# Performance work log

Hardware: AMD Instinct MI355X
Metric: run time of the kernel (lower is better)

The kernel has to match this reference:

```python
import jax, jax.numpy as jnp
import numpy as np

OUT = 7      # roi_align output_size
RATIO = 2    # fixed sampling_ratio (torchvision default -1 is adaptive; fixed 2 used for jit-ability)
IMG = 518    # image size (DINOv2 patch 14 -> 37x37 feature grid)


def setup_inputs() -> dict:
    key = jax.random.key(0)
    ks = jax.random.split(key, 12)
    B, N, C, H, W = 4, 512, 256, 37, 37
    NUM_CLASSES = 91
    f0 = jax.random.normal(ks[0], (B, C, H, W), jnp.float32)
    f1 = jax.random.normal(ks[1], (B, C, H, W), jnp.float32)
    f2 = jax.random.normal(ks[2], (B, C, H, W), jnp.float32)
    f3 = jax.random.normal(ks[3], (B, C, H, W), jnp.float32)
    # proposals in image coords so areas span all 4 level buckets (32^2..128^2+)
    cx = jax.random.uniform(ks[4], (B, N)) * IMG
    cy = jax.random.uniform(ks[5], (B, N)) * IMG
    bw = jax.random.uniform(ks[6], (B, N)) * 248.0 + 8.0
    bh = jax.random.uniform(ks[7], (B, N)) * 248.0 + 8.0
    x1 = jnp.maximum(cx - 0.5 * bw, 0.0)
    y1 = jnp.maximum(cy - 0.5 * bh, 0.0)
    x2 = jnp.minimum(cx + 0.5 * bw, float(IMG))
    y2 = jnp.minimum(cy + 0.5 * bh, float(IMG))
    proposals = jnp.stack([x1, y1, x2, y2], axis=-1)  # [B,N,4]
    D = C * OUT * OUT  # 12544
    w1 = jax.random.normal(ks[8], (D, 1024), jnp.float32) * 0.02
    b1 = jnp.zeros((1024,), jnp.float32)
    w2 = jax.random.normal(ks[9], (1024, 1024), jnp.float32) * 0.02
    b2 = jnp.zeros((1024,), jnp.float32)
    wc = jax.random.normal(ks[10], (1024, NUM_CLASSES), jnp.float32) * 0.02
    bc = jnp.zeros((NUM_CLASSES,), jnp.float32)
    wb = jax.random.normal(ks[11], (1024, 4), jnp.float32) * 0.02
    bb = jnp.zeros((4,), jnp.float32)
    return {"f0": f0, "f1": f1, "f2": f2, "f3": f3, "proposals": proposals,
            "w1": w1, "b1": b1, "w2": w2, "b2": b2,
            "wc": wc, "bc": bc, "wb": wb, "bb": bb}


def _multilevel_roi_align(f0, f1, f2, f3, proposals):
    B, C, H, W = f0.shape
    N = proposals.shape[1]
    P = OUT * RATIO * OUT * RATIO
    # levels stacked along spatial axis: [B, C, 4*H*W]
    feats_cat = jnp.stack([f0, f1, f2, f3], axis=2).reshape(B, C, 4 * H * W)
    bw = proposals[..., 2] - proposals[..., 0]
    bh = proposals[..., 3] - proposals[..., 1]
    area = bw * bh
    # area-based FPN level: <32^2->0, <64^2->1, <128^2->2, else 3
    lvl = ((area >= 32.0 ** 2).astype(jnp.int32)
           + (area >= 64.0 ** 2).astype(jnp.int32)
           + (area >= 128.0 ** 2).astype(jnp.int32))  # [B,N]
    # roi_align, spatial_scale=1.0, aligned=True
    x1 = proposals[..., 0] - 0.5
    y1 = proposals[..., 1] - 0.5
    bin_w = bw / OUT
    bin_h = bh / OUT
    offs = jnp.arange(OUT, dtype=jnp.float32)[:, None] + (jnp.arange(RATIO, dtype=jnp.float32) + 0.5)[None, :] / RATIO  # [7,2]
    ys = y1[..., None, None] + offs * bin_h[..., None, None]  # [B,N,7,2]
    xs = x1[..., None, None] + offs * bin_w[..., None, None]  # [B,N,7,2]
    y = ys[..., :, :, None, None]  # [B,N,7,2,1,1]
    x = xs[..., None, None, :, :]  # [B,N,1,1,7,2]
    valid = ((y >= -1.0) & (y <= H) & (x >= -1.0) & (x <= W)).astype(f0.dtype)
    yc = jnp.clip(y, 0.0, H - 1.0)
    xc = jnp.clip(x, 0.0, W - 1.0)
    y0f = jnp.floor(yc)
    x0f = jnp.floor(xc)
    y0 = y0f.astype(jnp.int32)
    x0 = x0f.astype(jnp.int32)
    y1i = jnp.minimum(y0 + 1, H - 1)
    x1i = jnp.minimum(x0 + 1, W - 1)
    ly = yc - y0f
    lx = xc - x0f
    hy = 1.0 - ly
    hx = 1.0 - lx
    base = (lvl * (H * W))[:, :, None, None, None, None]
    shp = (B, N, OUT, RATIO, OUT, RATIO)

    def gather(yi, xi):
        idx = jnp.broadcast_to(base + yi * W + xi, shp).reshape(B, N * P)
        return jax.vmap(lambda fb, ib: jnp.take(fb, ib, axis=1))(feats_cat, idx)  # [B,C,N*P]

    def wflat(w):
        return jnp.broadcast_to(w * valid, shp).reshape(B, 1, N * P)

    acc = (wflat(hy * hx) * gather(y0, x0)
           + wflat(hy * lx) * gather(y0, x1i)
           + wflat(ly * hx) * gather(y1i, x0)
           + wflat(ly * lx) * gather(y1i, x1i))
    roi = acc.reshape(B, C, N, OUT, RATIO, OUT, RATIO).sum(axis=(4, 6)) / (RATIO * RATIO)
    return roi.transpose(0, 2, 1, 3, 4)  # [B,N,C,7,7]


def reference(f0, f1, f2, f3, proposals, w1, b1, w2, b2, wc, bc, wb, bb):
    B, N = proposals.shape[0], proposals.shape[1]
    roi = _multilevel_roi_align(f0, f1, f2, f3, proposals)  # [B,N,C,7,7]
    flat = roi.reshape(B * N, -1)  # torch flatten order matches [C,7,7]
    h1 = jax.nn.relu(flat @ w1 + b1)
    h2 = jax.nn.relu(h1 @ w2 + b2)
    scores = (h2 @ wc + bc).reshape(B, N, -1)
    bbox_deltas = (h2 @ wb + bb).reshape(B, N, 4)
    return scores, bbox_deltas
```

## Files before the change

kernel.cpp:

```cpp
#include <hip/hip_runtime.h>
#include <hip/hip_bf16.h>
#include <stdint.h>

#define FH 37
#define FW 37
#define FC 256
#define NB 4
#define NP 512
#define BNT (NB*NP)
#define KDIM (FC*49)
#define HID 1024
#define NHEAD 95
#define CAP 256

typedef __bf16 bf16x8 __attribute__((ext_vector_type(8)));
typedef float  f32x4  __attribute__((ext_vector_type(4)));

__global__ __launch_bounds__(256) void k_transpose(const float* __restrict__ f0,
                                                   const float* __restrict__ f1,
                                                   const float* __restrict__ f2,
                                                   const float* __restrict__ f3,
                                                   float* __restrict__ ft) {
  __shared__ float tile[32][33];
  int bl = blockIdx.z;
  int b = bl >> 2, l = bl & 3;
  const float* src = (l == 0 ? f0 : l == 1 ? f1 : l == 2 ? f2 : f3) + (size_t)b * FC * FH * FW;
  int yx0 = blockIdx.x * 32;
  int c0  = blockIdx.y * 32;
  int tx = threadIdx.x;
  int ty = threadIdx.y;
  #pragma unroll
  for (int i = 0; i < 32; i += 8) {
    int c  = c0 + ty + i;
    int yx = yx0 + tx;
    float v = (yx < FH * FW) ? src[(size_t)c * (FH * FW) + yx] : 0.f;
    tile[ty + i][tx] = v;
  }
  __syncthreads();
  #pragma unroll
  for (int i = 0; i < 32; i += 8) {
    int yx = yx0 + ty + i;
    int c  = c0 + tx;
    if (yx < FH * FW)
      ft[((size_t)bl * (FH * FW) + yx) * FC + c] = tile[tx][ty + i];
  }
}

__global__ __launch_bounds__(256) void k_compact(const float* __restrict__ props,
                                                 int* __restrict__ count,
                                                 int* __restrict__ list) {
  int bn = blockIdx.x * 256 + threadIdx.x;
  float px1 = props[(size_t)bn * 4 + 0];
  float py1 = props[(size_t)bn * 4 + 1];
  float px2 = props[(size_t)bn * 4 + 2];
  float py2 = props[(size_t)bn * 4 + 3];
  float bw = px2 - px1, bh = py2 - py1;
  float X1 = px1 - 0.5f, Y1 = py1 - 0.5f;
  float binw = bw * (1.f / 7.f), binh = bh * (1.f / 7.f);
  float sy0 = Y1 + ((float)0 * 0.5f + 0.25f) * binh;
  float sx0 = X1 + ((float)0 * 0.5f + 0.25f) * binw;
  bool active = (sy0 <= 37.f) && (sx0 <= 37.f);
  if (active) {
    int s = atomicAdd(count, 1);
    if (s < CAP) list[s] = bn;
  }
}

__global__ __launch_bounds__(256) void k_roi(const float* __restrict__ ft,
                                             const float* __restrict__ props,
                                             const int* __restrict__ count,
                                             const int* __restrict__ list,
                                             __hip_bfloat16* __restrict__ Ahi,
                                             __hip_bfloat16* __restrict__ Alo) {
  int s = blockIdx.x;
  int cnt = min(*count, CAP);
  if (s >= cnt) return;
  int bn = list[s];
  int b = bn >> 9;
  int p = blockIdx.y;
  int oy = p / 7, ox = p % 7;
  int c = threadIdx.x;

  float px1 = props[(size_t)bn * 4 + 0];
  float py1 = props[(size_t)bn * 4 + 1];
  float px2 = props[(size_t)bn * 4 + 2];
  float py2 = props[(size_t)bn * 4 + 3];
  float bw = px2 - px1, bh = py2 - py1;
  float area = bw * bh;
  int lvl = (area >= 1024.f) + (area >= 4096.f) + (area >= 16384.f);
  float X1 = px1 - 0.5f, Y1 = py1 - 0.5f;
  float binw = bw * (1.f / 7.f), binh = bh * (1.f / 7.f);
  int fbase = ((b * 4 + lvl) * (FH * FW)) * FC;

  float acc = 0.f;
  #pragma unroll
  for (int ry = 0; ry < 2; ++ry) {
    int iy = oy * 2 + ry;
    float sy = Y1 + ((float)iy * 0.5f + 0.25f) * binh;
    #pragma unroll
    for (int rx = 0; rx < 2; ++rx) {
      int ix = ox * 2 + rx;
      float sx = X1 + ((float)ix * 0.5f + 0.25f) * binw;
      float valid = (sy >= -1.f && sy <= 37.f && sx >= -1.f && sx <= 37.f) ? 0.25f : 0.f;
      float yc = fminf(fmaxf(sy, 0.f), 36.f);
      float xc = fminf(fmaxf(sx, 0.f), 36.f);
      float y0f = floorf(yc), x0f = floorf(xc);
      int y0 = (int)y0f, x0 = (int)x0f;
      int y1i = min(y0 + 1, 36), x1i = min(x0 + 1, 36);
      float ly = yc - y0f, lx = xc - x0f;
      float hy = 1.f - ly, hx = 1.f - lx;
      float w00 = hy * hx * valid, w01 = hy * lx * valid;
      float w10 = ly * hx * valid, w11 = ly * lx * valid;
      if (w00 != 0.f) acc += w00 * ft[fbase + (y0  * FW + x0 ) * FC + c];
      if (w01 != 0.f) acc += w01 * ft[fbase + (y0  * FW + x1i) * FC + c];
      if (w10 != 0.f) acc += w10 * ft[fbase + (y1i * FW + x0 ) * FC + c];
      if (w11 != 0.f) acc += w11 * ft[fbase + (y1i * FW + x1i) * FC + c];
    }
  }
  size_t o = (size_t)s * KDIM + p * FC + c;
  __hip_bfloat16 h = __float2bfloat16(acc);
  Ahi[o] = h;
  Alo[o] = __float2bfloat16(acc - __bfloat162float(h));
}

__global__ __launch_bounds__(256, 2) void k_gemm_fused(
    const __hip_bfloat16* __restrict__ Ahi,
    const __hip_bfloat16* __restrict__ Alo,
    const float* __restrict__ Wf,
    float* __restrict__ part,
    const int* __restrict__ countPtr,
    int Kt, int kChunk, int reorder) {
  int cnt = min(*countPtr, CAP);
  if ((int)blockIdx.x * 128 >= cnt) return;
  __shared__ __align__(16) char lds[49152];
  const int t = threadIdx.x, lane = t & 63, wave = t >> 6;
  const int m0 = blockIdx.x * 128, n0 = blockIdx.y * 64;
  const int kStart = blockIdx.z * kChunk;
  const int niters = kChunk >> 5;

  const int nn = t & 63;
  const int q2 = t >> 6;
  const size_t rstep = reorder ? (size_t)(49 * HID) : (size_t)HID;

  const int wm = (wave & 1) * 64, wn2 = (wave >> 1) * 32;
  const int rsel = lane & 15, q = lane >> 4;

  f32x4 acc[4][2];
  #pragma unroll
  for (int m = 0; m < 4; ++m)
    #pragma unroll
    for (int n = 0; n < 2; ++n)
      acc[m][n] = (f32x4){0.f, 0.f, 0.f, 0.f};

  auto loadB = [&](float* v, int k0) {
    size_t rb0 = reorder ? (size_t)((k0 & 255) * 49 + (k0 >> 8)) : (size_t)k0;
    const float* p = Wf + rb0 * HID + (size_t)(q2 * 8) * rstep + n0 + nn;
    #pragma unroll
    for (int j = 0; j < 8; ++j) v[j] = p[(size_t)j * rstep];
  };

  auto writeB = [&](int buf, const float* v) {
    bf16x8 hv, lv;
    #pragma unroll
    for (int e = 0; e < 8; ++e) {
      float f = v[e];
      __hip_bfloat16 h = __float2bfloat16(f);
      float fr = f - __bfloat162float(h);
      __hip_bfloat16 l2 = __float2bfloat16(fr);
      hv[e] = *reinterpret_cast<__bf16*>(&h);
      lv[e] = *reinterpret_cast<__bf16*>(&l2);
    }
    char* bh = lds + buf * 24576 + 16384 + nn * 64 + ((q2 ^ (nn & 3)) << 4);
    *(bf16x8*)bh = hv;
    *(bf16x8*)(bh + 4096) = lv;
  };

  auto stageA = [&](int buf, int k0) {
    #pragma unroll
    for (int pl = 0; pl < 2; ++pl) {
      const __hip_bfloat16* src = pl ? Alo : Ahi;
      #pragma unroll
      for (int i = 0; i < 2; ++i) {
        int seg = wave * 2 + i;
        int row = seg * 16 + (lane >> 2);
        int cq = (lane & 3) ^ (row & 3);
        const char* g = (const char*)(src + (size_t)(m0 + row) * Kt + k0 + cq * 8);
        char* l = lds + buf * 24576 + pl * 8192 + seg * 1024;
        __builtin_amdgcn_global_load_lds((const unsigned int __attribute__((address_space(1)))*)g,
                                         (unsigned int __attribute__((address_space(3)))*)l,
                                         16, 0, 0);
      }
    }
  };

  auto compute = [&](int buf) {
    const char* base = lds + buf * 24576;
    bf16x8 ah[4], al2[4], bh2[2], bl2[2];
    #pragma unroll
    for (int mf = 0; mf < 4; ++mf) {
      int row = wm + mf * 16 + rsel;
      int off = row * 64 + ((q ^ (row & 3)) << 4);
      ah[mf]  = *(const bf16x8*)(base + off);
      al2[mf] = *(const bf16x8*)(base + 8192 + off);
    }
    #pragma unroll
    for (int nf = 0; nf < 2; ++nf) {
      int col = wn2 + nf * 16 + rsel;
      int off = col * 64 + ((q ^ (col & 3)) << 4);
      bh2[nf] = *(const bf16x8*)(base + 16384 + off);
      bl2[nf] = *(const bf16x8*)(base + 20480 + off);
    }
    #pragma unroll
    for (int mf = 0; mf < 4; ++mf)
      #pragma unroll
      for (int nf = 0; nf < 2; ++nf) {
        acc[mf][nf] = __builtin_amdgcn_mfma_f32_16x16x32_bf16(ah[mf],  bh2[nf], acc[mf][nf], 0, 0, 0);
        acc[mf][nf] = __builtin_amdgcn_mfma_f32_16x16x32_bf16(ah[mf],  bl2[nf], acc[mf][nf], 0, 0, 0);
        acc[mf][nf] = __builtin_amdgcn_mfma_f32_16x16x32_bf16(al2[mf], bh2[nf], acc[mf][nf], 0, 0, 0);
      }
  };

  float vA[8], vB[8];
  loadB(vA, kStart);
  stageA(0, kStart);
  writeB(0, vA);
  __syncthreads();

  int k = kStart;
  const int npair = niters >> 1;
  for (int pr = 0; pr < npair; ++pr) {
    loadB(vB, k + 32);
    stageA(1, k + 32);
    compute(0);
    writeB(1, vB);
    __syncthreads();
    bool more = (pr + 1 < npair);
    if (more) {
      loadB(vA, k + 64);
      stageA(0, k + 64);
    }
    compute(1);
    if (more) writeB(0, vA);
    __syncthreads();
    k += 64;
  }

  float* pbase = part + (size_t)blockIdx.z * (CAP * HID);
  #pragma unroll
  for (int mf = 0; mf < 4; ++mf)
    #pragma unroll
    for (int nf = 0; nf < 2; ++nf) {
      int row = m0 + wm + mf * 16 + q * 4;
      int col = n0 + wn2 + nf * 16 + rsel;
      #pragma unroll
      for (int r = 0; r < 4; ++r)
        pbase[(size_t)(row + r) * HID + col] = acc[mf][nf][r];
    }
}

__global__ __launch_bounds__(256) void k_reduce1(const float* __restrict__ part,
                                                 const float* __restrict__ bias,
                                                 const int* __restrict__ countPtr,
                                                 int S,
                                                 __hip_bfloat16* __restrict__ Hhi,
                                                 __hip_bfloat16* __restrict__ Hlo) {
  int cnt = min(*countPtr, CAP);
  if ((int)(blockIdx.x >> 2) >= cnt) return;
  size_t i = (size_t)blockIdx.x * 256 + threadIdx.x;
  const size_t tot = (size_t)CAP * HID;
  int col = (int)(i & (HID - 1));
  float a = bias[col];
  for (int s = 0; s < S; ++s) a += part[(size_t)s * tot + i];
  a = fmaxf(a, 0.f);
  __hip_bfloat16 h = __float2bfloat16(a);
  Hhi[i] = h;
  Hlo[i] = __float2bfloat16(a - __bfloat162float(h));
}

__global__ __launch_bounds__(256) void k_h2c(const float* __restrict__ w2,
                                             const float* __restrict__ b1,
                                             float* __restrict__ h2cr) {
  int n = blockIdx.x * 256 + threadIdx.x;
  int k0 = blockIdx.y * 128;
  float acc = 0.f;
  for (int k = k0; k < k0 + 128; ++k)
    acc += fmaxf(b1[k], 0.f) * w2[(size_t)k * HID + n];
  atomicAdd(&h2cr[n], acc);
}

__global__ __launch_bounds__(256) void k_outc(const float* __restrict__ h2cr,
                                              const float* __restrict__ b2,
                                              const float* __restrict__ wc,
                                              const float* __restrict__ bc,
                                              const float* __restrict__ wb,
                                              const float* __restrict__ bb,
                                              float* __restrict__ outc) {
  __shared__ float red[4];
  int j = blockIdx.x;
  int t = threadIdx.x;
  float acc = 0.f;
  for (int n = t; n < HID; n += 256) {
    float h = fmaxf(b2[n] + h2cr[n], 0.f);
    float w = (j < 91) ? wc[(size_t)n * 91 + j] : wb[(size_t)n * 4 + (j - 91)];
    acc += h * w;
  }
  #pragma unroll
  for (int o = 32; o; o >>= 1) acc += __shfl_down(acc, o, 64);
  if ((t & 63) == 0) red[t >> 6] = acc;
  __syncthreads();
  if (t == 0) {
    float bj = (j < 91) ? bc[j] : bb[j - 91];
    outc[j] = bj + red[0] + red[1] + red[2] + red[3];
  }
}

__global__ __launch_bounds__(256) void k_fill(const float* __restrict__ outc,
                                              float* __restrict__ out) {
  int i = blockIdx.x * 256 + threadIdx.x;
  const int SC = BNT * 91;
  if (i < SC) out[i] = outc[i % 91];
  else {
    int r = i - SC;
    if (r < BNT * 4) out[SC + r] = outc[91 + (r & 3)];
  }
}

__global__ __launch_bounds__(256) void k_head(const float* __restrict__ part,
                                              const float* __restrict__ b2,
                                              const float* __restrict__ wc,
                                              const float* __restrict__ bc,
                                              const float* __restrict__ wb,
                                              const float* __restrict__ bb,
                                              const int* __restrict__ count,
                                              const int* __restrict__ list,
                                              float* __restrict__ out) {
  __shared__ float row[HID];
  int s = blockIdx.x;
  int cnt = min(*count, CAP);
  if (s >= cnt) return;
  int bn = list[s];
  int t = threadIdx.x;
  const size_t tot = (size_t)CAP * HID;
  #pragma unroll
  for (int j = 0; j < 4; ++j) {
    int col = t + j * 256;
    float a = b2[col];
    #pragma unroll
    for (int ss = 0; ss < 8; ++ss) a += part[(size_t)ss * tot + (size_t)s * HID + col];
    row[col] = fmaxf(a, 0.f);
  }
  __syncthreads();
  if (t < NHEAD) {
    float acc = (t < 91) ? bc[t] : bb[t - 91];
    if (t < 91) {
      for (int k = 0; k < HID; ++k) acc += row[k] * wc[(size_t)k * 91 + t];
      out[(size_t)bn * 91 + t] = acc;
    } else {
      for (int k = 0; k < HID; ++k) acc += row[k] * wb[(size_t)k * 4 + (t - 91)];
      out[(size_t)BNT * 91 + (size_t)bn * 4 + (t - 91)] = acc;
    }
  }
}

extern "C" void kernel_launch(void* const* d_in, const int* in_sizes, int n_in,
                              void* d_out, int out_size, void* d_ws, size_t ws_size,
                              hipStream_t stream) {
  const float* f0    = (const float*)d_in[0];
  const float* f1    = (const float*)d_in[1];
  const float* f2    = (const float*)d_in[2];
  const float* f3    = (const float*)d_in[3];
  const float* props = (const float*)d_in[4];
  const float* w1    = (const float*)d_in[5];
  const float* b1    = (const float*)d_in[6];
  const float* w2    = (const float*)d_in[7];
  const float* b2    = (const float*)d_in[8];
  const float* wc    = (const float*)d_in[9];
  const float* bc    = (const float*)d_in[10];
  const float* wb    = (const float*)d_in[11];
  const float* bb    = (const float*)d_in[12];
  float* out = (float*)d_out;

  char* ws = (char*)d_ws;
  size_t off = 0;
  auto alloc = [&](size_t bytes) -> char* {
    char* p = ws + off;
    off += (bytes + 255) & ~(size_t)255;
    return p;
  };
  float*          ft    = (float*)         alloc((size_t)16 * FH * FW * FC * 4);
  __hip_bfloat16* Ahi   = (__hip_bfloat16*)alloc((size_t)CAP * KDIM * 2);
  __hip_bfloat16* Alo   = (__hip_bfloat16*)alloc((size_t)CAP * KDIM * 2);
  float*          part  = (float*)         alloc((size_t)28 * CAP * HID * 4);
  __hip_bfloat16* H1hi  = (__hip_bfloat16*)alloc((size_t)CAP * HID * 2);
  __hip_bfloat16* H1lo  = (__hip_bfloat16*)alloc((size_t)CAP * HID * 2);
  float*          h2cr  = (float*)         alloc(HID * 4);
  int*            count = (int*)           alloc(256);
  int*            list  = (int*)           alloc(CAP * 4);
  float*          outc  = (float*)         alloc(NHEAD * 4);
  (void)ws_size; (void)in_sizes; (void)n_in; (void)out_size;

  hipMemsetAsync(h2cr, 0, HID * 4 + 256, stream);

  k_transpose<<<dim3(43, 8, 16), dim3(32, 8), 0, stream>>>(f0, f1, f2, f3, ft);
  k_compact<<<8, 256, 0, stream>>>(props, count, list);
  k_roi<<<dim3(CAP, 49), 256, 0, stream>>>(ft, props, count, list, Ahi, Alo);

  k_h2c<<<dim3(4, 8), 256, 0, stream>>>(w2, b1, h2cr);
  k_outc<<<NHEAD, 256, 0, stream>>>(h2cr, b2, wc, bc, wb, bb, outc);
  k_fill<<<760, 256, 0, stream>>>(outc, out);

  k_gemm_fused<<<dim3(CAP / 128, 16, 28), 256, 0, stream>>>(Ahi, Alo, w1, part, count,
                                                            KDIM, 448, 1);
  k_reduce1<<<CAP * HID / 256, 256, 0, stream>>>(part, b1, count, 28, H1hi, H1lo);
  k_gemm_fused<<<dim3(CAP / 128, 16, 8), 256, 0, stream>>>(H1hi, H1lo, w2, part, count,
                                                           HID, 128, 0);
  k_head<<<CAP, 256, 0, stream>>>(part, b2, wc, bc, wb, bb, count, list, out);
}
```

Measured before the change: 240.3 us.

## Store ROI features in channel-major order and widen GEMM N-tile to 128

The ROI kernel now writes activations in [C,49] flatten order, so the first GEMM reads w1 rows contiguously and drops the strided reorder indexing of B loads. The GEMM block tile grows from 128x64 to 128x128, with each wave computing a 64x64 sub-tile and LDS doubled to 64KB. This halves the number of N blocks and raises A reuse per block, but it increases register pressure (16 accumulators, 16-value B prefetch) and LDS use, which may lower occupancy.

Measured after the change: 237.1 us. About the same (-1.4%).

```diff
diff --git a/kernel.cpp b/kernel.cpp
--- a/kernel.cpp
+++ b/kernel.cpp
@@ -117,7 +117,7 @@
       if (w11 != 0.f) acc += w11 * ft[fbase + (y1i * FW + x1i) * FC + c];
     }
   }
-  size_t o = (size_t)s * KDIM + p * FC + c;
+  size_t o = (size_t)s * KDIM + (size_t)c * 49 + p;
   __hip_bfloat16 h = __float2bfloat16(acc);
   Ahi[o] = h;
   Alo[o] = __float2bfloat16(acc - __bfloat162float(h));
@@ -129,50 +129,54 @@
     const float* __restrict__ Wf,
     float* __restrict__ part,
     const int* __restrict__ countPtr,
-    int Kt, int kChunk, int reorder) {
+    int Kt, int kChunk) {
   int cnt = min(*countPtr, CAP);
   if ((int)blockIdx.x * 128 >= cnt) return;
-  __shared__ __align__(16) char lds[49152];
+  __shared__ __align__(16) char lds[65536];
   const int t = threadIdx.x, lane = t & 63, wave = t >> 6;
-  const int m0 = blockIdx.x * 128, n0 = blockIdx.y * 64;
+  const int m0 = blockIdx.x * 128, n0 = blockIdx.y * 128;
   const int kStart = blockIdx.z * kChunk;
   const int niters = kChunk >> 5;
 
-  const int nn = t & 63;
-  const int q2 = t >> 6;
-  const size_t rstep = reorder ? (size_t)(49 * HID) : (size_t)HID;
-
-  const int wm = (wave & 1) * 64, wn2 = (wave >> 1) * 32;
+  const int nn = t & 127;
+  const int kq = t >> 7;
+
+  const int wm = (wave >> 1) * 64, wn = (wave & 1) * 64;
   const int rsel = lane & 15, q = lane >> 4;
 
-  f32x4 acc[4][2];
+  f32x4 acc[4][4];
   #pragma unroll
   for (int m = 0; m < 4; ++m)
     #pragma unroll
-    for (int n = 0; n < 2; ++n)
+    for (int n = 0; n < 4; ++n)
       acc[m][n] = (f32x4){0.f, 0.f, 0.f, 0.f};
 
   auto loadB = [&](float* v, int k0) {
-    size_t rb0 = reorder ? (size_t)((k0 & 255) * 49 + (k0 >> 8)) : (size_t)k0;
-    const float* p = Wf + rb0 * HID + (size_t)(q2 * 8) * rstep + n0 + nn;
-    #pragma unroll
-    for (int j = 0; j < 8; ++j) v[j] = p[(size_t)j * rstep];
+    const float* p = Wf + (size_t)(k0 + kq * 16) * HID + n0 + nn;
+    #pragma unroll
+    for (int j = 0; j < 16; ++j) v[j] = p[(size_t)j * HID];
   };
 
   auto writeB = [&](int buf, const float* v) {
-    bf16x8 hv, lv;
-    #pragma unroll
-    for (int e = 0; e < 8; ++e) {
-      float f = v[e];
-      __hip_bfloat16 h = __float2bfloat16(f);
-      float fr = f - __bfloat162float(h);
-      __hip_bfloat16 l2 = __float2bfloat16(fr);
-      hv[e] = *reinterpret_cast<__bf16*>(&h);
-      lv[e] = *reinterpret_cast<__bf16*>(&l2);
-    }
-    char* bh = lds + buf * 24576 + 16384 + nn * 64 + ((q2 ^ (nn & 3)) << 4);
-    *(bf16x8*)bh = hv;
-    *(bf16x8*)(bh + 4096) = lv;
+    char* bh = lds + buf * 32768 + 16384;
+    char* bl = lds + buf * 32768 + 24576;
+    #pragma unroll
+    for (int hh = 0; hh < 2; ++hh) {
+      bf16x8 hv, lv;
+      #pragma unroll
+      for (int e = 0; e < 8; ++e) {
+        float f = v[hh * 8 + e];
+        __hip_bfloat16 h = __float2bfloat16(f);
+        float fr = f - __bfloat162float(h);
+        __hip_bfloat16 l2 = __float2bfloat16(fr);
+        hv[e] = *reinterpret_cast<__bf16*>(&h);
+        lv[e] = *reinterpret_cast<__bf16*>(&l2);
+      }
+      int oct = kq * 2 + hh;
+      int off = nn * 64 + ((oct ^ (nn & 3)) << 4);
+      *(bf16x8*)(bh + off) = hv;
+      *(bf16x8*)(bl + off) = lv;
+    }
   };
 
   auto stageA = [&](int buf, int k0) {
@@ -185,7 +189,7 @@
         int row = seg * 16 + (lane >> 2);
         int cq = (lane & 3) ^ (row & 3);
         const char* g = (const char*)(src + (size_t)(m0 + row) * Kt + k0 + cq * 8);
-        char* l = lds + buf * 24576 + pl * 8192 + seg * 1024;
+        char* l = lds + buf * 32768 + pl * 8192 + seg * 1024;
         __builtin_amdgcn_global_load_lds((const unsigned int __attribute__((address_space(1)))*)g,
                                          (unsigned int __attribute__((address_space(3)))*)l,
                                          16, 0, 0);
@@ -194,8 +198,8 @@
   };
 
   auto compute = [&](int buf) {
-    const char* base = lds + buf * 24576;
-    bf16x8 ah[4], al2[4], bh2[2], bl2[2];
+    const char* base = lds + buf * 32768;
+    bf16x8 ah[4], al2[4], bh2[4], bl2[4];
     #pragma unroll
     for (int mf = 0; mf < 4; ++mf) {
       int row = wm + mf * 16 + rsel;
@@ -204,23 +208,23 @@
       al2[mf] = *(const bf16x8*)(base + 8192 + off);
     }
     #pragma unroll
-    for (int nf = 0; nf < 2; ++nf) {
-      int col = wn2 + nf * 16 + rsel;
+    for (int nf = 0; nf < 4; ++nf) {
+      int col = wn + nf * 16 + rsel;
       int off = col * 64 + ((q ^ (col & 3)) << 4);
       bh2[nf] = *(const bf16x8*)(base + 16384 + off);
-      bl2[nf] = *(const bf16x8*)(base + 20480 + off);
+      bl2[nf] = *(const bf16x8*)(base + 24576 + off);
     }
     #pragma unroll
     for (int mf = 0; mf < 4; ++mf)
       #pragma unroll
-      for (int nf = 0; nf < 2; ++nf) {
+      for (int nf = 0; nf < 4; ++nf) {
         acc[mf][nf] = __builtin_amdgcn_mfma_f32_16x16x32_bf16(ah[mf],  bh2[nf], acc[mf][nf], 0, 0, 0);
         acc[mf][nf] = __builtin_amdgcn_mfma_f32_16x16x32_bf16(ah[mf],  bl2[nf], acc[mf][nf], 0, 0, 0);
         acc[mf][nf] = __builtin_amdgcn_mfma_f32_16x16x32_bf16(al2[mf], bh2[nf], acc[mf][nf], 0, 0, 0);
       }
   };
 
-  float vA[8], vB[8];
+  float vA[16], vB[16];
   loadB(vA, kStart);
   stageA(0, kStart);
   writeB(0, vA);
@@ -249,9 +253,9 @@
   #pragma unroll
   for (int mf = 0; mf < 4; ++mf)
     #pragma unroll
-    for (int nf = 0; nf < 2; ++nf) {
+    for (int nf = 0; nf < 4; ++nf) {
       int row = m0 + wm + mf * 16 + q * 4;
-      int col = n0 + wn2 + nf * 16 + rsel;
+      int col = n0 + wn + nf * 16 + rsel;
       #pragma unroll
       for (int r = 0; r < 4; ++r)
         pbase[(size_t)(row + r) * HID + col] = acc[mf][nf][r];
@@ -409,10 +413,10 @@
   k_outc<<<NHEAD, 256, 0, stream>>>(h2cr, b2, wc, bc, wb, bb, outc);
   k_fill<<<760, 256, 0, stream>>>(outc, out);
 
-  k_gemm_fused<<<dim3(CAP / 128, 16, 28), 256, 0, stream>>>(Ahi, Alo, w1, part, count,
-                                                            KDIM, 448, 1);
+  k_gemm_fused<<<dim3(CAP / 128, 8, 28), 256, 0, stream>>>(Ahi, Alo, w1, part, count,
+                                                           KDIM, 448);
   k_reduce1<<<CAP * HID / 256, 256, 0, stream>>>(part, b1, count, 28, H1hi, H1lo);
-  k_gemm_fused<<<dim3(CAP / 128, 16, 8), 256, 0, stream>>>(H1hi, H1lo, w2, part, count,
-                                                           HID, 128, 0);
+  k_gemm_fused<<<dim3(CAP / 128, 8, 8), 256, 0, stream>>>(H1hi, H1lo, w2, part, count,
+                                                          HID, 128);
   k_head<<<CAP, 256, 0, stream>>>(part, b2, wc, bc, wb, bb, count, list, out);
 }
```
